# Optimization experiments

Measured on AMD Instinct MI355X. Metric: run time of the kernel, lower is better.

## Reference

```python
import jax, jax.numpy as jnp
import numpy as np

D_MODEL = 4096
NUM_EXPERTS = 16
HID_PER_EXPERT = 11008 // NUM_EXPERTS  # 688
NUM_SELECTS = 4
BALANCE_WEIGHT = 0.01
CV_EPS = 1e-10


def setup_inputs() -> dict:
    key = jax.random.key(0)
    ks = jax.random.split(key, 5)
    x = jax.random.normal(ks[0], (2, 2048, D_MODEL), dtype=jnp.float32)
    # gate network: Linear(input_size, num_experts, bias=False); stored as [D, E] for x @ W
    w_gate_net = jax.random.normal(ks[1], (D_MODEL, NUM_EXPERTS), dtype=jnp.float32) * (1.0 / np.sqrt(D_MODEL))
    # per-expert GLU weights (torch Linear convention [out, in]), stacked over experts
    s = 1.0 / np.sqrt(D_MODEL)
    w_g = jax.random.normal(ks[2], (NUM_EXPERTS, HID_PER_EXPERT, D_MODEL), dtype=jnp.float32) * s
    w_u = jax.random.normal(ks[3], (NUM_EXPERTS, HID_PER_EXPERT, D_MODEL), dtype=jnp.float32) * s
    w_d = jax.random.normal(ks[4], (NUM_EXPERTS, D_MODEL, HID_PER_EXPERT), dtype=jnp.float32) * (1.0 / np.sqrt(HID_PER_EXPERT))
    return {"x": x, "w_gate_net": w_gate_net, "w_g": w_g, "w_u": w_u, "w_d": w_d}


def _cv_squared(v):
    v = v.astype(jnp.float32)
    return jnp.var(v, ddof=1) / (jnp.mean(v) ** 2 + CV_EPS)


def reference(x, w_gate_net, w_g, w_u, w_d):
    B, S, D = x.shape
    E = w_g.shape[0]
    xt = x.reshape(-1, D)                      # [T, D]
    T = xt.shape[0]

    # --- TopKBalancedNoisyGate (eval path: no noise) ---
    logits = xt @ w_gate_net                   # [T, E]
    top_logits, top_idx = jax.lax.top_k(logits, NUM_SELECTS)   # [T, K]
    scores = jax.nn.softmax(top_logits.astype(jnp.float32), axis=-1).astype(logits.dtype)
    combine = jnp.zeros((T, E), dtype=logits.dtype)
    combine = combine.at[jnp.arange(T)[:, None], top_idx].set(scores)  # scatter topK scores
    importance = combine.sum(axis=0)           # [E]
    load = (combine > 0).sum(axis=0).astype(jnp.float32)
    balance_loss = (_cv_squared(importance) + _cv_squared(load)) * BALANCE_WEIGHT

    # --- UniversalCalculator with LinearGLUExperts (silu GLU, no bias) ---
    # dense per-expert compute; unrouted tokens have combine weight 0, so math matches
    # the gather/grouped-GEMM/scatter of the original exactly.
    g = jnp.einsum('td,ehd->teh', xt, w_g)     # [T, E, Hper]
    u = jnp.einsum('td,ehd->teh', xt, w_u)
    h = jax.nn.silu(g) * u * combine[:, :, None]  # multiply_gate_scores before down proj (bias-free => exact)
    y = jnp.einsum('teh,edh->td', h, w_d)      # [T, D]
    return y.reshape(B, S, -1), balance_loss
```

## Files before the change

### kernel.cpp

```cpp
#include <hip/hip_runtime.h>
#include <hip/hip_bf16.h>

#define D_MODEL 4096
#define NEXP    16
#define HID     688
#define HIDP    704
#define NSEL    4
#define NTOK    4096

typedef __attribute__((ext_vector_type(4))) float  f32x4;
typedef __attribute__((ext_vector_type(8))) short  bf16x8;

__device__ __forceinline__ short f2bf(float f) {
  __hip_bfloat16 h = __float2bfloat16(f);
  return __builtin_bit_cast(short, h);
}

__device__ __forceinline__ float bf2f(short s) {
  const unsigned u = ((unsigned)(unsigned short)s) << 16;
  return __builtin_bit_cast(float, u);
}

__device__ __forceinline__ void gload16(const void* g, void* l) {
  __builtin_amdgcn_global_load_lds(
      (const __attribute__((address_space(1))) unsigned int*)g,
      (__attribute__((address_space(3))) unsigned int*)l, 16, 0, 0);
}

__global__ void zero_meta_kernel(int* counts, float* importance) {
  const int tid = threadIdx.x;
  if (tid < NEXP) counts[tid] = 0;
  else if (tid < 2 * NEXP) importance[tid - NEXP] = 0.f;
}

__global__ void zero_y_kernel(float* __restrict__ y) {
  const size_t i = (size_t)blockIdx.x * 256 + threadIdx.x;
  *(f32x4*)(y + i * 4) = f32x4{0.f, 0.f, 0.f, 0.f};
}

__global__ __launch_bounds__(256) void gate_conv_kernel(
    const float* __restrict__ x, const float* __restrict__ wg,
    int* __restrict__ counts, float* __restrict__ importance,
    int* __restrict__ pair_tok, float* __restrict__ pair_scr,
    int* __restrict__ pair_rank, short* __restrict__ xb,
    const float* __restrict__ w_g, const float* __restrict__ w_u,
    short* __restrict__ gb, short* __restrict__ ub,
    const float* __restrict__ w_d, short* __restrict__ wdb)
{
  __shared__ double red[4][NEXP];
  const int tid = threadIdx.x;
  const int r4  = blockIdx.x & 3;
  const int b4  = blockIdx.x >> 2;

  if (r4 == 0) {
    const size_t stride = (size_t)2048 * 256;
    const size_t n8 = (size_t)NEXP * HIDP * (D_MODEL / 8);
    for (size_t i = (size_t)b4 * 256 + tid; i < n8; i += stride) {
      const int c8  = (int)(i & 511);
      const int row = (int)((i >> 9) % HIDP);
      const int e   = (int)(i / (512 * HIDP));
      bf16x8 og, ou;
      if (row < HID) {
        const size_t so = ((size_t)e * HID + row) * D_MODEL + (size_t)c8 * 8;
        const f32x4 ga  = *(const f32x4*)(w_g + so);
        const f32x4 gbv = *(const f32x4*)(w_g + so + 4);
        const f32x4 ua  = *(const f32x4*)(w_u + so);
        const f32x4 ubv = *(const f32x4*)(w_u + so + 4);
        #pragma unroll
        for (int j = 0; j < 4; ++j) {
          og[j] = f2bf(ga[j]); og[4 + j] = f2bf(gbv[j]);
          ou[j] = f2bf(ua[j]); ou[4 + j] = f2bf(ubv[j]);
        }
      } else {
        #pragma unroll
        for (int j = 0; j < 8; ++j) { og[j] = 0; ou[j] = 0; }
      }
      *(bf16x8*)(gb + i * 8) = og;
      *(bf16x8*)(ub + i * 8) = ou;
    }
    return;
  }

  if (r4 == 1) {
    const size_t stride = (size_t)2048 * 256;
    const size_t n8 = (size_t)NEXP * D_MODEL * (HIDP / 8);
    for (size_t i = (size_t)b4 * 256 + tid; i < n8; i += stride) {
      const int c8  = (int)(i % 88);
      const int row = (int)((i / 88) & (D_MODEL - 1));
      const int e   = (int)(i / (88 * D_MODEL));
      bf16x8 o;
      if (c8 < 86) {
        const size_t so = ((size_t)e * D_MODEL + row) * HID + (size_t)c8 * 8;
        const f32x4 a = *(const f32x4*)(w_d + so);
        const f32x4 b = *(const f32x4*)(w_d + so + 4);
        #pragma unroll
        for (int j = 0; j < 4; ++j) { o[j] = f2bf(a[j]); o[4 + j] = f2bf(b[j]); }
      } else {
        #pragma unroll
        for (int j = 0; j < 8; ++j) o[j] = 0;
      }
      *(bf16x8*)(wdb + i * 8) = o;
    }
    return;
  }

  const int t = b4 * 2 + (r4 - 2);
  const float* xr = x + (size_t)t * D_MODEL;
  {
    short* xbr = xb + (size_t)t * D_MODEL;
    for (int i8 = tid; i8 < D_MODEL / 8; i8 += 256) {
      const f32x4 a = *(const f32x4*)(xr + i8 * 8);
      const f32x4 b = *(const f32x4*)(xr + i8 * 8 + 4);
      bf16x8 o;
      #pragma unroll
      for (int j = 0; j < 4; ++j) { o[j] = f2bf(a[j]); o[4 + j] = f2bf(b[j]); }
      *(bf16x8*)(xbr + i8 * 8) = o;
    }
  }

  double acc[NEXP];
  #pragma unroll
  for (int e = 0; e < NEXP; ++e) acc[e] = 0.0;

  for (int i = tid; i < D_MODEL; i += 256) {
    const float xv = xr[i];
    const f32x4* w = (const f32x4*)(wg + (size_t)i * NEXP);
    #pragma unroll
    for (int q = 0; q < 4; ++q) {
      const f32x4 wv = w[q];
      #pragma unroll
      for (int j = 0; j < 4; ++j) acc[q * 4 + j] += (double)xv * (double)wv[j];
    }
  }

  #pragma unroll
  for (int e = 0; e < NEXP; ++e) {
    double v = acc[e];
    #pragma unroll
    for (int off = 32; off > 0; off >>= 1) v += __shfl_xor(v, off, 64);
    acc[e] = v;
  }

  const int lane = tid & 63, wid = tid >> 6;
  if (lane == 0) {
    #pragma unroll
    for (int e = 0; e < NEXP; ++e) red[wid][e] = acc[e];
  }
  __syncthreads();

  if (tid == 0) {
    float lg[NEXP];
    #pragma unroll
    for (int e = 0; e < NEXP; ++e)
      lg[e] = (float)(red[0][e] + red[1][e] + red[2][e] + red[3][e]);

    int   idx[NSEL];
    float val[NSEL];
    unsigned used = 0;
    for (int k = 0; k < NSEL; ++k) {
      float best = -3.4e38f; int bi = 0;
      for (int e = 0; e < NEXP; ++e)
        if (!((used >> e) & 1u) && lg[e] > best) { best = lg[e]; bi = e; }
      idx[k] = bi; val[k] = best; used |= 1u << bi;
    }
    const float m = val[0];
    float ex[NSEL], s = 0.f;
    for (int k = 0; k < NSEL; ++k) { ex[k] = expf(val[k] - m); s += ex[k]; }
    for (int k = 0; k < NSEL; ++k) {
      const float sc = ex[k] / s;
      const int e = idx[k];
      const int pos = atomicAdd(&counts[e], 1);
      pair_tok[e * NTOK + pos]  = t;
      pair_scr[e * NTOK + pos]  = sc;
      pair_rank[e * NTOK + pos] = k;
      atomicAdd(&importance[e], sc);
    }
  }
}

__global__ void scan_loss_kernel(const int* __restrict__ counts,
                                 const float* __restrict__ importance,
                                 int* __restrict__ offs, float* __restrict__ loss_out)
{
  if (threadIdx.x != 0 || blockIdx.x != 0) return;
  int   c[NEXP]; float im[NEXP];
  for (int e = 0; e < NEXP; ++e) { c[e] = counts[e]; im[e] = importance[e]; }
  int o = 0;
  for (int e = 0; e < NEXP; ++e) { offs[e] = o; o += c[e]; }
  float mi = 0.f, ml = 0.f;
  for (int e = 0; e < NEXP; ++e) { mi += im[e]; ml += (float)c[e]; }
  mi /= NEXP; ml /= NEXP;
  float vi = 0.f, vl = 0.f;
  for (int e = 0; e < NEXP; ++e) {
    vi += (im[e] - mi) * (im[e] - mi);
    vl += ((float)c[e] - ml) * ((float)c[e] - ml);
  }
  vi /= (NEXP - 1); vl /= (NEXP - 1);
  const float loss = 0.01f * (vi / (mi * mi + 1e-10f) + vl / (ml * ml + 1e-10f));
  *loss_out = loss;
}

__global__ __launch_bounds__(256, 4) void stage1b_kernel(
    const short* __restrict__ xb, const short* __restrict__ wgb,
    const short* __restrict__ wub, const int* __restrict__ counts,
    const int* __restrict__ offs, const int* __restrict__ pair_tok,
    const float* __restrict__ pair_scr, short* __restrict__ H)
{
  const int bid = blockIdx.x;
  const int ht  = bid >> 9;
  const int q   = bid & 511;
  const int xcd = q & 7;
  const int idx = q >> 3;
  const int e   = xcd * 2 + (idx & 1);
  const int mt  = idx >> 1;

  const int n_e = counts[e];
  const int m0  = mt * 128;
  if (m0 >= n_e) return;
  const int h0  = ht * 64;

  __shared__ short ldsA[2][128 * 32];
  __shared__ short ldsG[2][64 * 32];
  __shared__ short ldsU[2][64 * 32];

  const int tid  = threadIdx.x;
  const int lane = tid & 63;
  const int wid  = tid >> 6;

  const short* srcA[2]; const short* srcG; const short* srcU;
  #pragma unroll
  for (int i = 0; i < 2; ++i) {
    const int c    = wid * 2 + i;
    const int row  = 16 * c + (lane >> 2);
    const int slot = (lane & 3) ^ ((row >> 1) & 3);
    int r = m0 + row; if (r >= n_e) r = n_e - 1;
    const int tok = pair_tok[e * NTOK + r];
    srcA[i] = xb + (size_t)tok * D_MODEL + slot * 8;
  }
  {
    const int row  = 16 * wid + (lane >> 2);
    const int slot = (lane & 3) ^ ((row >> 1) & 3);
    const size_t rb = ((size_t)e * HIDP + h0 + row) * D_MODEL + slot * 8;
    srcG = wgb + rb;
    srcU = wub + rb;
  }

  const int wm = wid >> 1, wn = wid & 1;
  const int fr = lane & 15, fs = lane >> 4;
  const int so = (fs ^ ((fr >> 1) & 3)) * 8;

  f32x4 accg[4][2], accu[4][2];
  #pragma unroll
  for (int fi = 0; fi < 4; ++fi)
    #pragma unroll
    for (int fj = 0; fj < 2; ++fj) {
      accg[fi][fj] = f32x4{0.f, 0.f, 0.f, 0.f};
      accu[fi][fj] = f32x4{0.f, 0.f, 0.f, 0.f};
    }

  auto stage = [&](int kt, int b) {
    const int ko = kt * 32;
    #pragma unroll
    for (int i = 0; i < 2; ++i)
      gload16(srcA[i] + ko, &ldsA[b][(wid * 2 + i) * 512]);
    gload16(srcG + ko, &ldsG[b][wid * 512]);
    gload16(srcU + ko, &ldsU[b][wid * 512]);
  };

  auto compute = [&](int b) {
    const short* Ab = ldsA[b]; const short* Gb = ldsG[b]; const short* Ub = ldsU[b];
    bf16x8 af[4], bg[2], bu[2];
    #pragma unroll
    for (int fi = 0; fi < 4; ++fi)
      af[fi] = *(const bf16x8*)&Ab[(wm * 64 + fi * 16 + fr) * 32 + so];
    #pragma unroll
    for (int fj = 0; fj < 2; ++fj) {
      bg[fj] = *(const bf16x8*)&Gb[(wn * 32 + fj * 16 + fr) * 32 + so];
      bu[fj] = *(const bf16x8*)&Ub[(wn * 32 + fj * 16 + fr) * 32 + so];
    }
    #pragma unroll
    for (int fi = 0; fi < 4; ++fi)
      #pragma unroll
      for (int fj = 0; fj < 2; ++fj) {
        accg[fi][fj] = __builtin_amdgcn_mfma_f32_16x16x32_bf16(af[fi], bg[fj], accg[fi][fj], 0, 0, 0);
        accu[fi][fj] = __builtin_amdgcn_mfma_f32_16x16x32_bf16(af[fi], bu[fj], accu[fi][fj], 0, 0, 0);
      }
  };

  const int KT = D_MODEL / 32;
  stage(0, 0);
  for (int kt = 0; kt < KT; ++kt) {
    const int cur = kt & 1;
    __syncthreads();
    if (kt + 1 < KT) stage(kt + 1, cur ^ 1);
    compute(cur);
  }

  const int offs_e = offs[e];
  #pragma unroll
  for (int fi = 0; fi < 4; ++fi)
    #pragma unroll
    for (int fj = 0; fj < 2; ++fj)
      #pragma unroll
      for (int j = 0; j < 4; ++j) {
        const int r = m0 + wm * 64 + fi * 16 + fs * 4 + j;
        if (r < n_e) {
          const int c = h0 + wn * 32 + fj * 16 + fr;
          const float sc = pair_scr[e * NTOK + r];
          const float g  = accg[fi][fj][j];
          const float u  = accu[fi][fj][j];
          const float hv = (g / (1.f + expf(-g))) * u * sc;
          H[(size_t)(offs_e + r) * HIDP + c] = f2bf(hv);
        }
      }
}

__global__ __launch_bounds__(512, 4) void stage2s_kernel(
    const short* __restrict__ H, const short* __restrict__ wdb,
    const int* __restrict__ counts, const int* __restrict__ offs,
    const int* __restrict__ pair_tok, const int* __restrict__ pair_rank,
    short* __restrict__ Yk)
{
  const int bid = blockIdx.x;
  const int dt  = bid >> 9;
  const int q   = bid & 511;
  const int xcd = q & 7;
  const int idx = q >> 3;
  const int e   = xcd * 2 + (idx & 1);
  const int mt  = idx >> 1;

  const int n_e = counts[e];
  const int m0  = mt * 128;
  if (m0 >= n_e) return;
  const int d0  = dt * 256;

  __shared__ short ldsA[2][128 * 32];
  __shared__ short ldsB[2][256 * 32];

  const int tid  = threadIdx.x;
  const int lane = tid & 63;
  const int wv   = tid >> 6;
  const int offs_e = offs[e];

  const short* srcA; const short* srcB[2];
  {
    const int row  = tid >> 2;
    const int slot = (tid & 3) ^ ((row >> 1) & 3);
    int r = m0 + row; if (r >= n_e) r = n_e - 1;
    srcA = H + (size_t)(offs_e + r) * HIDP + slot * 8;
  }
  #pragma unroll
  for (int i = 0; i < 2; ++i) {
    const int row  = i * 128 + (tid >> 2);
    const int slot = (tid & 3) ^ ((row >> 1) & 3);
    srcB[i] = wdb + ((size_t)e * D_MODEL + d0 + row) * HIDP + slot * 8;
  }

  const int wm = wv >> 2, wn = wv & 3;
  const int fr = lane & 15, fs = lane >> 4;
  const int so = (fs ^ ((fr >> 1) & 3)) * 8;

  f32x4 acc[4][4];
  #pragma unroll
  for (int fi = 0; fi < 4; ++fi)
    #pragma unroll
    for (int fj = 0; fj < 4; ++fj) acc[fi][fj] = f32x4{0.f, 0.f, 0.f, 0.f};

  auto stage = [&](int kt, int b) {
    const int ko = kt * 32;
    gload16(srcA + ko, &ldsA[b][wv * 512]);
    #pragma unroll
    for (int i = 0; i < 2; ++i)
      gload16(srcB[i] + ko, &ldsB[b][i * 4096 + wv * 512]);
  };

  auto compute = [&](int b) {
    const short* Ab = ldsA[b]; const short* Bb = ldsB[b];
    bf16x8 af[4], bb[4];
    #pragma unroll
    for (int fi = 0; fi < 4; ++fi)
      af[fi] = *(const bf16x8*)&Ab[(wm * 64 + fi * 16 + fr) * 32 + so];
    #pragma unroll
    for (int fj = 0; fj < 4; ++fj)
      bb[fj] = *(const bf16x8*)&Bb[(wn * 64 + fj * 16 + fr) * 32 + so];
    #pragma unroll
    for (int fi = 0; fi < 4; ++fi)
      #pragma unroll
      for (int fj = 0; fj < 4; ++fj)
        acc[fi][fj] = __builtin_amdgcn_mfma_f32_16x16x32_bf16(af[fi], bb[fj], acc[fi][fj], 0, 0, 0);
  };

  const int KT = HIDP / 32;
  stage(0, 0);
  for (int kt = 0; kt < KT; ++kt) {
    const int cur = kt & 1;
    __syncthreads();
    if (kt + 1 < KT) stage(kt + 1, cur ^ 1);
    compute(cur);
  }

  #pragma unroll
  for (int fi = 0; fi < 4; ++fi)
    #pragma unroll
    for (int j = 0; j < 4; ++j) {
      const int r = m0 + wm * 64 + fi * 16 + fs * 4 + j;
      if (r < n_e) {
        const int tok = pair_tok[e * NTOK + r];
        const int rk  = pair_rank[e * NTOK + r];
        short* yr = Yk + ((size_t)rk * NTOK + tok) * D_MODEL + d0 + wn * 64 + fr;
        #pragma unroll
        for (int fj = 0; fj < 4; ++fj)
          yr[fj * 16] = f2bf(acc[fi][fj][j]);
      }
    }
}

__global__ __launch_bounds__(256) void reduce_y_kernel(const short* __restrict__ Yk,
                                                       float* __restrict__ y) {
  const size_t i = ((size_t)blockIdx.x * 256 + threadIdx.x) * 8;
  const size_t P = (size_t)NTOK * D_MODEL;
  const bf16x8 a = *(const bf16x8*)(Yk + i);
  const bf16x8 b = *(const bf16x8*)(Yk + P + i);
  const bf16x8 c = *(const bf16x8*)(Yk + 2 * P + i);
  const bf16x8 d = *(const bf16x8*)(Yk + 3 * P + i);
  f32x4 lo, hi;
  #pragma unroll
  for (int j = 0; j < 4; ++j) {
    lo[j] = bf2f(a[j]) + bf2f(b[j]) + bf2f(c[j]) + bf2f(d[j]);
    hi[j] = bf2f(a[4 + j]) + bf2f(b[4 + j]) + bf2f(c[4 + j]) + bf2f(d[4 + j]);
  }
  *(f32x4*)(y + i)     = lo;
  *(f32x4*)(y + i + 4) = hi;
}

__global__ __launch_bounds__(256, 4) void stage2a_kernel(
    const short* __restrict__ H, const short* __restrict__ wdb,
    const int* __restrict__ counts, const int* __restrict__ offs,
    const int* __restrict__ pair_tok, float* __restrict__ y)
{
  const int bid = blockIdx.x;
  const int dt  = bid >> 9;
  const int q   = bid & 511;
  const int xcd = q & 7;
  const int idx = q >> 3;
  const int e   = xcd * 2 + (idx & 1);
  const int mt  = idx >> 1;

  const int n_e = counts[e];
  const int m0  = mt * 128;
  if (m0 >= n_e) return;
  const int d0  = dt * 128;

  __shared__ short ldsA[2][128 * 32];
  __shared__ short ldsB[2][128 * 32];

  const int tid  = threadIdx.x;
  const int lane = tid & 63;
  const int wid  = tid >> 6;
  const int offs_e = offs[e];

  const short* srcA[2]; const short* srcB[2];
  #pragma unroll
  for (int i = 0; i < 2; ++i) {
    const int c    = wid * 2 + i;
    const int row  = 16 * c + (lane >> 2);
    const int slot = (lane & 3) ^ ((row >> 1) & 3);
    int r = m0 + row; if (r >= n_e) r = n_e - 1;
    srcA[i] = H + (size_t)(offs_e + r) * HIDP + slot * 8;
    srcB[i] = wdb + ((size_t)e * D_MODEL + d0 + row) * HIDP + slot * 8;
  }

  const int wm = wid >> 1, wn = wid & 1;
  const int fr = lane & 15, fs = lane >> 4;
  const int so = (fs ^ ((fr >> 1) & 3)) * 8;

  f32x4 acc[4][4];
  #pragma unroll
  for (int fi = 0; fi < 4; ++fi)
    #pragma unroll
    for (int fj = 0; fj < 4; ++fj) acc[fi][fj] = f32x4{0.f, 0.f, 0.f, 0.f};

  auto stage = [&](int kt, int b) {
    const int ko = kt * 32;
    #pragma unroll
    for (int i = 0; i < 2; ++i) {
      gload16(srcA[i] + ko, &ldsA[b][(wid * 2 + i) * 512]);
      gload16(srcB[i] + ko, &ldsB[b][(wid * 2 + i) * 512]);
    }
  };

  auto compute = [&](int b) {
    const short* Ab = ldsA[b]; const short* Bb = ldsB[b];
    bf16x8 af[4], bb[4];
    #pragma unroll
    for (int fi = 0; fi < 4; ++fi)
      af[fi] = *(const bf16x8*)&Ab[(wm * 64 + fi * 16 + fr) * 32 + so];
    #pragma unroll
    for (int fj = 0; fj < 4; ++fj)
      bb[fj] = *(const bf16x8*)&Bb[(wn * 64 + fj * 16 + fr) * 32 + so];
    #pragma unroll
    for (int fi = 0; fi < 4; ++fi)
      #pragma unroll
      for (int fj = 0; fj < 4; ++fj)
        acc[fi][fj] = __builtin_amdgcn_mfma_f32_16x16x32_bf16(af[fi], bb[fj], acc[fi][fj], 0, 0, 0);
  };

  const int KT = HIDP / 32;
  stage(0, 0);
  for (int kt = 0; kt < KT; ++kt) {
    const int cur = kt & 1;
    __syncthreads();
    if (kt + 1 < KT) stage(kt + 1, cur ^ 1);
    compute(cur);
  }

  #pragma unroll
  for (int fi = 0; fi < 4; ++fi)
    #pragma unroll
    for (int j = 0; j < 4; ++j) {
      const int r = m0 + wm * 64 + fi * 16 + fs * 4 + j;
      if (r < n_e) {
        const int tok = pair_tok[e * NTOK + r];
        float* yr = y + (size_t)tok * D_MODEL + d0 + wn * 64 + fr;
        #pragma unroll
        for (int fj = 0; fj < 4; ++fj)
          atomicAdd(yr + fj * 16, acc[fi][fj][j]);
      }
    }
}

extern "C" void kernel_launch(void* const* d_in, const int* in_sizes, int n_in,
                              void* d_out, int out_size, void* d_ws, size_t ws_size,
                              hipStream_t stream) {
  const float* x     = (const float*)d_in[0];
  const float* wgate = (const float*)d_in[1];
  const float* w_g   = (const float*)d_in[2];
  const float* w_u   = (const float*)d_in[3];
  const float* w_d   = (const float*)d_in[4];

  float* y        = (float*)d_out;
  float* loss_out = y + (size_t)NTOK * D_MODEL;

  char* ws = (char*)d_ws;
  int*   counts     = (int*)ws;
  int*   offs       = counts + 16;
  float* importance = (float*)(counts + 32);
  int*   pair_tok   = (int*)(ws + 256);
  float* pair_scr   = (float*)(ws + 256 + (size_t)NEXP * NTOK * 4);
  int*   pair_rank  = (int*)(ws + 256 + (size_t)2 * NEXP * NTOK * 4);
  short* H          = (short*)(ws + 256 + (size_t)3 * NEXP * NTOK * 4);

  const size_t H_BYTES = (size_t)NTOK * NSEL * HIDP * 2;
  short* xbuf = (short*)((char*)H + H_BYTES);
  short* wgb  = xbuf + (size_t)NTOK * D_MODEL;
  short* wub  = wgb + (size_t)NEXP * HIDP * D_MODEL;
  short* wdb  = wub + (size_t)NEXP * HIDP * D_MODEL;
  short* Yk   = wdb + (size_t)NEXP * HIDP * D_MODEL;

  const size_t NEED_STORE = ((char*)(Yk + (size_t)NSEL * NTOK * D_MODEL)) - ws;
  const bool store_path = ws_size >= NEED_STORE;

  hipLaunchKernelGGL(zero_meta_kernel, dim3(1), dim3(64), 0, stream, counts, importance);
  hipLaunchKernelGGL(gate_conv_kernel, dim3(8192), dim3(256), 0, stream,
                     x, wgate, counts, importance, pair_tok, pair_scr, pair_rank, xbuf,
                     w_g, w_u, wgb, wub, w_d, wdb);
  hipLaunchKernelGGL(scan_loss_kernel, dim3(1), dim3(64), 0, stream,
                     counts, importance, offs, loss_out);
  hipLaunchKernelGGL(stage1b_kernel, dim3(11 * 512), dim3(256), 0, stream,
                     xbuf, wgb, wub, counts, offs, pair_tok, pair_scr, H);

  if (store_path) {
    hipLaunchKernelGGL(stage2s_kernel, dim3(16 * 512), dim3(512), 0, stream,
                       H, wdb, counts, offs, pair_tok, pair_rank, Yk);
    hipLaunchKernelGGL(reduce_y_kernel, dim3(NTOK * D_MODEL / 8 / 256), dim3(256), 0, stream,
                       Yk, y);
  } else {
    hipLaunchKernelGGL(zero_y_kernel, dim3(16384), dim3(256), 0, stream, y);
    hipLaunchKernelGGL(stage2a_kernel, dim3(32 * 512), dim3(256), 0, stream,
                       H, wdb, counts, offs, pair_tok, y);
  }
}
```

Before: 750.4 us.

## Deepen weight prefetch to three LDS stages with explicit vmcnt waits

Both grouped GEMM kernels now split staging into activation and weight loads. Weights are triple-buffered and prefetched two k-steps ahead, while activations stay double-buffered one step ahead. The __syncthreads calls are replaced with raw s_barrier plus manual s_waitcnt vmcnt counts, so waits cover only the buffer about to be consumed. This is meant to hide global-load latency for the weight streams, at the cost of extra LDS and fragile hand-counted vmcnt values.

```diff
diff --git a/kernel.cpp b/kernel.cpp
--- a/kernel.cpp
+++ b/kernel.cpp
@@ -10,6 +10,8 @@
 
 typedef __attribute__((ext_vector_type(4))) float  f32x4;
 typedef __attribute__((ext_vector_type(8))) short  bf16x8;
+
+#define VMCNT(n) asm volatile("s_waitcnt vmcnt(" #n ")" ::: "memory")
 
 __device__ __forceinline__ short f2bf(float f) {
   __hip_bfloat16 h = __float2bfloat16(f);
@@ -220,8 +222,8 @@
   const int h0  = ht * 64;
 
   __shared__ short ldsA[2][128 * 32];
-  __shared__ short ldsG[2][64 * 32];
-  __shared__ short ldsU[2][64 * 32];
+  __shared__ short ldsG[3][64 * 32];
+  __shared__ short ldsU[3][64 * 32];
 
   const int tid  = threadIdx.x;
   const int lane = tid & 63;
@@ -258,17 +260,20 @@
       accu[fi][fj] = f32x4{0.f, 0.f, 0.f, 0.f};
     }
 
-  auto stage = [&](int kt, int b) {
+  auto stageA = [&](int kt, int b) {
     const int ko = kt * 32;
     #pragma unroll
     for (int i = 0; i < 2; ++i)
       gload16(srcA[i] + ko, &ldsA[b][(wid * 2 + i) * 512]);
+  };
+  auto stageGU = [&](int kt, int b) {
+    const int ko = kt * 32;
     gload16(srcG + ko, &ldsG[b][wid * 512]);
     gload16(srcU + ko, &ldsU[b][wid * 512]);
   };
 
-  auto compute = [&](int b) {
-    const short* Ab = ldsA[b]; const short* Gb = ldsG[b]; const short* Ub = ldsU[b];
+  auto compute = [&](int ab, int gub) {
+    const short* Ab = ldsA[ab]; const short* Gb = ldsG[gub]; const short* Ub = ldsU[gub];
     bf16x8 af[4], bg[2], bu[2];
     #pragma unroll
     for (int fi = 0; fi < 4; ++fi)
@@ -288,12 +293,21 @@
   };
 
   const int KT = D_MODEL / 32;
-  stage(0, 0);
+  stageGU(0, 0); stageGU(1, 1); stageA(0, 0);
+  int gub = 0;
   for (int kt = 0; kt < KT; ++kt) {
-    const int cur = kt & 1;
-    __syncthreads();
-    if (kt + 1 < KT) stage(kt + 1, cur ^ 1);
-    compute(cur);
+    const int ab = kt & 1;
+    __builtin_amdgcn_s_barrier();
+    __builtin_amdgcn_sched_barrier(0);
+    if (kt + 1 < KT) stageA(kt + 1, (kt + 1) & 1);
+    if (kt + 2 < KT) { int t3 = gub + 2; if (t3 >= 3) t3 -= 3; stageGU(kt + 2, t3); }
+    if (kt + 2 < KT)      { VMCNT(6); }
+    else if (kt + 1 < KT) { VMCNT(4); }
+    else                  { VMCNT(0); }
+    __builtin_amdgcn_s_barrier();
+    __builtin_amdgcn_sched_barrier(0);
+    compute(ab, gub);
+    ++gub; if (gub == 3) gub = 0;
   }
 
   const int offs_e = offs[e];
@@ -335,7 +349,7 @@
   const int d0  = dt * 256;
 
   __shared__ short ldsA[2][128 * 32];
-  __shared__ short ldsB[2][256 * 32];
+  __shared__ short ldsB[3][256 * 32];
 
   const int tid  = threadIdx.x;
   const int lane = tid & 63;
@@ -366,16 +380,18 @@
     #pragma unroll
     for (int fj = 0; fj < 4; ++fj) acc[fi][fj] = f32x4{0.f, 0.f, 0.f, 0.f};
 
-  auto stage = [&](int kt, int b) {
+  auto stageA = [&](int kt, int b) {
+    gload16(srcA + kt * 32, &ldsA[b][wv * 512]);
+  };
+  auto stageB = [&](int kt, int b) {
     const int ko = kt * 32;
-    gload16(srcA + ko, &ldsA[b][wv * 512]);
     #pragma unroll
     for (int i = 0; i < 2; ++i)
       gload16(srcB[i] + ko, &ldsB[b][i * 4096 + wv * 512]);
   };
 
-  auto compute = [&](int b) {
-    const short* Ab = ldsA[b]; const short* Bb = ldsB[b];
+  auto compute = [&](int ab, int bb_) {
+    const short* Ab = ldsA[ab]; const short* Bb = ldsB[bb_];
     bf16x8 af[4], bb[4];
     #pragma unroll
     for (int fi = 0; fi < 4; ++fi)
@@ -391,12 +407,21 @@
   };
 
   const int KT = HIDP / 32;
-  stage(0, 0);
+  stageB(0, 0); stageB(1, 1); stageA(0, 0);
+  int bb = 0;
   for (int kt = 0; kt < KT; ++kt) {
-    const int cur = kt & 1;
-    __syncthreads();
-    if (kt + 1 < KT) stage(kt + 1, cur ^ 1);
-    compute(cur);
+    const int ab = kt & 1;
+    __builtin_amdgcn_s_barrier();
+    __builtin_amdgcn_sched_barrier(0);
+    if (kt + 1 < KT) stageA(kt + 1, (kt + 1) & 1);
+    if (kt + 2 < KT) { int t3 = bb + 2; if (t3 >= 3) t3 -= 3; stageB(kt + 2, t3); }
+    if (kt + 2 < KT)      { VMCNT(5); }
+    else if (kt + 1 < KT) { VMCNT(3); }
+    else                  { VMCNT(0); }
+    __builtin_amdgcn_s_barrier();
+    __builtin_amdgcn_sched_barrier(0);
+    compute(ab, bb);
+    ++bb; if (bb == 3) bb = 0;
   }
 
   #pragma unroll
```

Result: slower. 765.6 us (+2.0%).
